# Kernel tuning notes

Hardware: AMD Instinct MI355X
Metric: run time of the kernel (lower is better)

## Reference

```python
import jax, jax.numpy as jnp
import numpy as np

NUM_NODES = 100000
NUM_EDGES = 1600000
FEAT = 128
HID = 128
NUM_GRAPHS = 512


def setup_inputs() -> dict:
    key = jax.random.key(0)
    ks = jax.random.split(key, 8)
    x = jax.random.normal(ks[0], (NUM_NODES, FEAT), dtype=jnp.float32)
    edge_index = jax.random.randint(ks[1], (2, NUM_EDGES), 0, NUM_NODES, dtype=jnp.int64)
    batch = jnp.sort(jax.random.randint(ks[2], (NUM_NODES,), 0, NUM_GRAPHS, dtype=jnp.int64))
    # Glorot-ish init for weights (scale named for clarity)
    s1 = 1.0 / np.sqrt(FEAT)
    s2 = 1.0 / np.sqrt(HID)
    W1 = jax.random.normal(ks[3], (FEAT, HID), dtype=jnp.float32) * s1
    b1 = jnp.zeros((HID,), dtype=jnp.float32)
    W2 = jax.random.normal(ks[4], (HID, HID), dtype=jnp.float32) * s2
    b2 = jnp.zeros((HID,), dtype=jnp.float32)
    Wout = jax.random.normal(ks[5], (HID, 1), dtype=jnp.float32) * s2
    bout = jnp.zeros((1,), dtype=jnp.float32)
    return {"x": x, "edge_index": edge_index, "batch": batch,
            "W1": W1, "b1": b1, "W2": W2, "b2": b2, "Wout": Wout, "bout": bout}


def reference(x, edge_index, batch, W1, b1, W2, b2, Wout, bout):
    N = x.shape[0]
    # PyG GCNConv: add self-loops, symmetric normalization D^-1/2 (A+I) D^-1/2
    loops = jnp.arange(N, dtype=edge_index.dtype)
    src = jnp.concatenate([edge_index[0], loops])  # [E+N]
    dst = jnp.concatenate([edge_index[1], loops])  # [E+N]
    ones = jnp.ones_like(dst, dtype=x.dtype)
    deg = jax.ops.segment_sum(ones, dst, num_segments=N)  # in-degree incl. self-loop
    dinv = jnp.where(deg > 0, jax.lax.rsqrt(deg), 0.0)
    coeff = (dinv[src] * dinv[dst])[:, None]  # [E+N, 1]

    def gcn(h, W, b):
        h = h @ W                                       # [N, H] dense GEMM
        msg = h[src] * coeff                            # gather + scale
        agg = jax.ops.segment_sum(msg, dst, num_segments=N)  # scatter-add
        return agg + b

    h = jax.nn.relu(gcn(x, W1, b1))
    h = jax.nn.relu(gcn(h, W2, b2))

    # global_mean_pool over batch ids
    G = NUM_GRAPHS
    sums = jax.ops.segment_sum(h, batch, num_segments=G)
    cnts = jax.ops.segment_sum(jnp.ones((N,), dtype=h.dtype), batch, num_segments=G)
    pooled = sums / jnp.maximum(cnts, 1.0)[:, None]

    return pooled @ Wout + bout  # [G, 1]
```

## Files before the change

kernel.cpp:

```cpp
#include <hip/hip_runtime.h>
#include <hip/hip_bf16.h>
#include <hip/hip_fp16.h>

#define FEAT 128
#define PSLOTS 64
#define BCAP 5120
#define NBIN 1024

typedef _Float16 h8 __attribute__((ext_vector_type(8)));
typedef float f4 __attribute__((ext_vector_type(4)));
typedef float fx2 __attribute__((ext_vector_type(2)));


__device__ __forceinline__ void wt_body(const float* __restrict__ W1,
                                        const float* __restrict__ W2,
                                        __half* __restrict__ Wt1,
                                        __half* __restrict__ Wt2, int bid) {
    int t = bid * 256 + threadIdx.x;
    const float* W = (t < 8192) ? W1 : W2;
    __half* Wt     = (t < 8192) ? Wt1 : Wt2;
    int u = t & 8191;
    int n = u >> 6, k2 = (u & 63) * 2;
    float a = W[(size_t)k2 * 128 + n];
    float b = W[(size_t)(k2 + 1) * 128 + n];
    ((__half2*)Wt)[n * 64 + (k2 >> 1)] = __floats2half2_rn(a, b);
}

__device__ __forceinline__ void bin_body(const int* __restrict__ ei, int E, int chunk,
                                         int* __restrict__ cursor,
                                         unsigned* __restrict__ binned, int nb,
                                         int bid, int* smem) {
    int* hist = smem;
    int* base = smem + 512;
    int start = bid * chunk;
    int end = start + chunk; if (end > E) end = E;
    for (int i = threadIdx.x; i < nb; i += 256) hist[i] = 0;
    __syncthreads();
    for (int e = start + threadIdx.x; e < end; e += 256)
        atomicAdd(&hist[ei[E + e] >> 8], 1);
    __syncthreads();
    for (int i = threadIdx.x; i < nb; i += 256) {
        int h = hist[i];
        base[i] = h ? atomicAdd(&cursor[i], h) : 0;
    }
    __syncthreads();
    for (int e = start + threadIdx.x; e < end; e += 256) {
        int s = ei[e];
        int d = ei[E + e];
        int b = d >> 8;
        int pos = atomicAdd(&base[b], 1);
        if (pos < BCAP)
            binned[(size_t)b * BCAP + pos] = (unsigned)s | ((unsigned)(d & 255) << 17);
    }
}

__global__ __launch_bounds__(256) void bin_wt(const int* __restrict__ ei, int E, int chunk,
                                              int* __restrict__ cursor,
                                              unsigned* __restrict__ binned, int nb,
                                              const float* __restrict__ W1,
                                              const float* __restrict__ W2,
                                              __half* __restrict__ Wt1,
                                              __half* __restrict__ Wt2) {
    __shared__ int smem[1024];
    if ((int)blockIdx.x < NBIN)
        bin_body(ei, E, chunk, cursor, binned, nb, blockIdx.x, smem);
    else
        wt_body(W1, W2, Wt1, Wt2, blockIdx.x - NBIN);
}


__device__ __forceinline__ void loadA(const __half* p, int quad, h8* a) {
#pragma unroll
    for (int ks = 0; ks < 4; ++ks)
        a[ks] = *(const h8*)(p + ks * 32 + quad * 8);
}
__device__ __forceinline__ void loadA(const float* p, int quad, h8* a) {
#pragma unroll
    for (int ks = 0; ks < 4; ++ks) {
        const float* q = p + ks * 32 + quad * 8;
        float4 f0 = *(const float4*)q;
        float4 f1 = *(const float4*)(q + 4);
        h8 v;
        v[0] = (_Float16)f0.x; v[1] = (_Float16)f0.y;
        v[2] = (_Float16)f0.z; v[3] = (_Float16)f0.w;
        v[4] = (_Float16)f1.x; v[5] = (_Float16)f1.y;
        v[6] = (_Float16)f1.z; v[7] = (_Float16)f1.w;
        a[ks] = v;
    }
}

template <typename TIN>
__device__ __forceinline__ void gemm_body(const TIN* __restrict__ X,
                                          const __half* __restrict__ Wt,
                                          unsigned char* __restrict__ Y, int N,
                                          const float* __restrict__ scale,
                                          int bid, _Float16* Bs) {
    {
        const float4* src = (const float4*)Wt;
        float4* dst = (float4*)Bs;
        for (int i = threadIdx.x; i < 2048; i += 256) {
            int n = i >> 4, ch = i & 15;
            dst[n * 16 + (ch ^ (n & 15))] = src[i];
        }
    }
    __syncthreads();

    int lane = threadIdx.x & 63;
    int wave = threadIdx.x >> 6;
    int m = lane & 15;
    int quad = lane >> 4;
    int rowb = bid * 128 + wave * 16;

    h8 a[2][4];
#pragma unroll
    for (int rt = 0; rt < 2; ++rt) {
        int rA = rowb + rt * 64 + m; if (rA >= N) rA = N - 1;
        loadA(X + (size_t)rA * FEAT, quad, a[rt]);
    }

    f4 acc[2][8];
#pragma unroll
    for (int rt = 0; rt < 2; ++rt)
#pragma unroll
        for (int nt = 0; nt < 8; ++nt) acc[rt][nt] = (f4){0.f, 0.f, 0.f, 0.f};

#pragma unroll
    for (int nt = 0; nt < 8; ++nt) {
        const _Float16* bbase = Bs + (nt * 16 + m) * 128;
#pragma unroll
        for (int ks = 0; ks < 4; ++ks) {
            int ch = (ks * 4 + quad) ^ m;
            h8 bfrag = *(const h8*)(bbase + ch * 8);
            acc[0][nt] = __builtin_amdgcn_mfma_f32_16x16x32_f16(a[0][ks], bfrag, acc[0][nt], 0, 0, 0);
            acc[1][nt] = __builtin_amdgcn_mfma_f32_16x16x32_f16(a[1][ks], bfrag, acc[1][nt], 0, 0, 0);
        }
    }

#pragma unroll
    for (int rt = 0; rt < 2; ++rt)
#pragma unroll
    for (int r = 0; r < 4; ++r) {
        int row = rowb + rt * 64 + quad * 4 + r;
        if (row < N) {
            float sc = scale[row];
#pragma unroll
            for (int nt = 0; nt < 8; ++nt) {
                float v = sc * acc[rt][nt][r];
                int pk = __builtin_amdgcn_cvt_pk_fp8_f32(v, v, 0, false);
                Y[(size_t)row * FEAT + nt * 16 + m] = (unsigned char)(pk & 0xFF);
            }
        }
    }
}

template <typename TIN>
__global__ __launch_bounds__(256) void gemm_mfma(const TIN* __restrict__ X,
                                                 const __half* __restrict__ Wt,
                                                 unsigned char* __restrict__ Y, int N,
                                                 const float* __restrict__ scale) {
    __shared__ __align__(16) _Float16 Bs[128 * 128];
    gemm_body<TIN>(X, Wt, Y, N, scale, blockIdx.x, Bs);
}


__global__ __launch_bounds__(256) void k_deg_fill(const unsigned* __restrict__ binned,
                                                  const int* __restrict__ cursor,
                                                  int N, int* __restrict__ deg,
                                                  int* __restrict__ rowstart,
                                                  float* __restrict__ dinv,
                                                  int* __restrict__ meta) {
    __shared__ int ld[256];
    __shared__ int sc[256];
    __shared__ int cur[256];
    int b = blockIdx.x;
    int cnt = cursor[b]; if (cnt > BCAP) cnt = BCAP;
    int s = b * BCAP, e = s + cnt;
    ld[threadIdx.x] = 0;
    __syncthreads();
    for (int i = s + threadIdx.x; i < e; i += 256)
        atomicAdd(&ld[binned[i] >> 17], 1);
    __syncthreads();
    int d = ld[threadIdx.x];
    sc[threadIdx.x] = d;
    __syncthreads();
    for (int off = 1; off < 256; off <<= 1) {
        int t = (threadIdx.x >= off) ? sc[threadIdx.x - off] : 0;
        __syncthreads();
        sc[threadIdx.x] += t;
        __syncthreads();
    }
    int rs = s + sc[threadIdx.x] - d;
    cur[threadIdx.x] = rs;
    int v = (b << 8) + threadIdx.x;
    if (v < N) {
        deg[v] = d;
        rowstart[v] = rs;
        dinv[v] = rsqrtf((float)d + 1.0f);
    }
    __syncthreads();
    for (int i = s + threadIdx.x; i < e; i += 256) {
        unsigned p = binned[i];
        int src = (int)(p & 0x1FFFF);
        int drl = (int)(p >> 17);
        int pos = atomicAdd(&cur[drl], 1);
        meta[pos] = src << 7;
    }
}


template <bool POOL>
__global__ __launch_bounds__(256) void agg_relu(const unsigned char* __restrict__ Y,
                                                const float* __restrict__ dinv,
                                                const int* __restrict__ rowstart,
                                                const int* __restrict__ degc,
                                                const int* __restrict__ meta,
                                                const float* __restrict__ bias,
                                                __half* __restrict__ H, int N,
                                                const float* __restrict__ Wout,
                                                const int* __restrict__ batch,
                                                float* __restrict__ gsum, int G) {
    int wid  = (blockIdx.x * 256 + threadIdx.x) >> 6;
    int lane = threadIdx.x & 63;
    if (wid >= N) return;
    int v = wid;
    float dv = dinv[v];
    int zoff = N << 7;

    const char* Yb = (const char*)Y;
    int lb = lane * 2;

    fx2 yv = __builtin_amdgcn_cvt_pk_f32_fp8(
        (int)*(const unsigned short*)(Y + (size_t)v * FEAT + lb), false);
    float accx = yv.x;
    float accy = yv.y;

    int base = rowstart[v];
    int n = degc[v];
    for (int i0 = 0; i0 < n; i0 += 64) {
        int m = n - i0; if (m > 64) m = 64;
        int sl = (lane < m) ? meta[base + i0 + lane] : zoff;
        for (int i = 0; i < m; i += 16) {
            int o[16];
            unsigned short u[16];
#pragma unroll
            for (int j = 0; j < 16; ++j) o[j] = __shfl(sl, i + j);
#pragma unroll
            for (int j = 0; j < 16; ++j)
                u[j] = *(const unsigned short*)(Yb + o[j] + lb);
#pragma unroll
            for (int j = 0; j < 16; ++j) {
                fx2 y = __builtin_amdgcn_cvt_pk_f32_fp8((int)u[j], false);
                accx += y.x;
                accy += y.y;
            }
        }
    }
    float2 b = ((const float2*)bias)[lane];
    float hx = fmaxf(dv * accx + b.x, 0.f);
    float hy = fmaxf(dv * accy + b.y, 0.f);
    if (POOL) {
        float2 wo = ((const float2*)Wout)[lane];
        float s = hx * wo.x + hy * wo.y;
        s += __shfl_xor(s, 1);
        s += __shfl_xor(s, 2);
        s += __shfl_xor(s, 4);
        s += __shfl_xor(s, 8);
        s += __shfl_xor(s, 16);
        s += __shfl_xor(s, 32);
        if (lane == 0) {
            int slot = blockIdx.x & (PSLOTS - 1);
            atomicAdd(&gsum[slot * G + batch[v]], s);
        }
    } else {
        ((__half2*)(H + (size_t)v * FEAT))[lane] = __floats2half2_rn(hx, hy);
    }
}


__global__ __launch_bounds__(256) void k_head(const float* __restrict__ gsum,
                                              const int* __restrict__ batch, int N, int G,
                                              const float* __restrict__ bout,
                                              float* __restrict__ out) {
    int g = blockIdx.x * 256 + threadIdx.x;
    if (g >= G) return;
    float s = 0.f;
#pragma unroll 8
    for (int k = 0; k < PSLOTS; ++k) s += gsum[k * G + g];
    int lo = 0, hi = N;
    while (lo < hi) { int mid = (lo + hi) >> 1; if (batch[mid] < g) lo = mid + 1; else hi = mid; }
    int start = lo;
    lo = start; hi = N;
    while (lo < hi) { int mid = (lo + hi) >> 1; if (batch[mid] < g + 1) lo = mid + 1; else hi = mid; }
    int cnt = lo - start;
    out[g] = s / (float)(cnt > 0 ? cnt : 1) + bout[0];
}


extern "C" void kernel_launch(void* const* d_in, const int* in_sizes, int n_in,
                              void* d_out, int out_size, void* d_ws, size_t ws_size,
                              hipStream_t stream) {
    const float* x    = (const float*)d_in[0];
    const int*   ei   = (const int*)d_in[1];
    const int*   batch= (const int*)d_in[2];
    const float* W1   = (const float*)d_in[3];
    const float* b1   = (const float*)d_in[4];
    const float* W2   = (const float*)d_in[5];
    const float* b2   = (const float*)d_in[6];
    const float* Wout = (const float*)d_in[7];
    const float* bout = (const float*)d_in[8];

    int N = in_sizes[0] / FEAT;
    int E = in_sizes[1] / 2;
    int G = out_size;
    int nb = (N + 255) >> 8;

    char* ws = (char*)d_ws;
    size_t off = 0;
    auto alloc = [&](size_t bytes) -> void* {
        void* p = ws + off;
        off += (bytes + 255) & ~(size_t)255;
        return p;
    };
    unsigned char* bufY = (unsigned char*)alloc((size_t)(N + 1) * FEAT);
    __half* bufH     = (__half*)alloc((size_t)N * FEAT * 2);
    __half* Wt1      = (__half*)alloc((size_t)FEAT * FEAT * 2);
    __half* Wt2      = (__half*)alloc((size_t)FEAT * FEAT * 2);
    float* dinv      = (float*)alloc((size_t)N * 4);
    int*   deg       = (int*)alloc((size_t)N * 4);
    int*   rowstart  = (int*)alloc((size_t)N * 4);
    float* gsum      = (float*)alloc((size_t)PSLOTS * G * 4 + (size_t)nb * 4);
    int*   cursor    = (int*)(gsum + (size_t)PSLOTS * G);
    unsigned* binned = (unsigned*)alloc((size_t)nb * BCAP * 4);
    int*   meta      = (int*)alloc((size_t)nb * BCAP * 4);

    int gemm_grid = (N + 127) / 128;
    int agg_grid  = (N + 3) / 4;
    int chunk = (E + NBIN - 1) / NBIN;

    hipMemsetAsync(gsum, 0, (size_t)PSLOTS * G * 4 + (size_t)nb * 4, stream);
    hipMemsetAsync(bufY + (size_t)N * FEAT, 0, FEAT, stream);
    bin_wt<<<NBIN + 64, 256, 0, stream>>>(ei, E, chunk, cursor, binned, nb,
                                          W1, W2, Wt1, Wt2);
    k_deg_fill<<<nb, 256, 0, stream>>>(binned, cursor, N, deg, rowstart, dinv, meta);
    gemm_mfma<float><<<gemm_grid, 256, 0, stream>>>(x, Wt1, bufY, N, dinv);
    agg_relu<false><<<agg_grid, 256, 0, stream>>>(bufY, dinv, rowstart, deg, meta, b1, bufH, N,
                                                  nullptr, nullptr, nullptr, 0);
    gemm_mfma<__half><<<gemm_grid, 256, 0, stream>>>(bufH, Wt2, bufY, N, dinv);
    agg_relu<true><<<agg_grid, 256, 0, stream>>>(bufY, dinv, rowstart, deg, meta, b2, nullptr, N,
                                                 Wout, batch, gsum, G);
    k_head<<<(G + 255) / 256, 256, 0, stream>>>(gsum, batch, N, G, bout, (float*)d_out);
}
```

Before: 290.7 us.

## Compute degrees with global atomics and overlap edge binning with first GEMM

A new pre-kernel computes node in-degrees with global atomics, transposes the weights and zeroes the padding row. This lets the first GEMM scale by rsqrt(deg+1) directly, so it runs in the same launch as edge binning and the two can overlap. k_deg_fill now reads deg instead of recounting per-bin histograms and pads meta with zero-row offsets. The aggregation kernel is restructured so four lane groups each gather 8-byte fp8 chunks for different neighbours and then reduce across groups with shuffles. The cost is one extra launch and a pass of global atomics over all edges.

```diff
diff --git a/kernel.cpp b/kernel.cpp
--- a/kernel.cpp
+++ b/kernel.cpp
@@ -6,6 +6,7 @@
 #define PSLOTS 64
 #define BCAP 5120
 #define NBIN 1024
+#define NDEG 1024
 
 typedef _Float16 h8 __attribute__((ext_vector_type(8)));
 typedef float f4 __attribute__((ext_vector_type(4)));
@@ -26,6 +27,27 @@
     ((__half2*)Wt)[n * 64 + (k2 >> 1)] = __floats2half2_rn(a, b);
 }
 
+
+__global__ __launch_bounds__(256) void k_pre(const int* __restrict__ ei, int E, int chunk,
+                                             int* __restrict__ deg,
+                                             const float* __restrict__ W1,
+                                             const float* __restrict__ W2,
+                                             __half* __restrict__ Wt1,
+                                             __half* __restrict__ Wt2,
+                                             unsigned char* __restrict__ padrow) {
+    int bid = blockIdx.x;
+    if (bid < NDEG) {
+        int start = bid * chunk;
+        int end = start + chunk; if (end > E) end = E;
+        for (int e = start + threadIdx.x; e < end; e += 256)
+            atomicAdd(&deg[ei[E + e]], 1);
+    } else if (bid < NDEG + 64) {
+        wt_body(W1, W2, Wt1, Wt2, bid - NDEG);
+    } else {
+        if (threadIdx.x < 8) ((uint4*)padrow)[threadIdx.x] = make_uint4(0, 0, 0, 0);
+    }
+}
+
 __device__ __forceinline__ void bin_body(const int* __restrict__ ei, int E, int chunk,
                                          int* __restrict__ cursor,
                                          unsigned* __restrict__ binned, int nb,
@@ -52,20 +74,6 @@
         if (pos < BCAP)
             binned[(size_t)b * BCAP + pos] = (unsigned)s | ((unsigned)(d & 255) << 17);
     }
-}
-
-__global__ __launch_bounds__(256) void bin_wt(const int* __restrict__ ei, int E, int chunk,
-                                              int* __restrict__ cursor,
-                                              unsigned* __restrict__ binned, int nb,
-                                              const float* __restrict__ W1,
-                                              const float* __restrict__ W2,
-                                              __half* __restrict__ Wt1,
-                                              __half* __restrict__ Wt2) {
-    __shared__ int smem[1024];
-    if ((int)blockIdx.x < NBIN)
-        bin_body(ei, E, chunk, cursor, binned, nb, blockIdx.x, smem);
-    else
-        wt_body(W1, W2, Wt1, Wt2, blockIdx.x - NBIN);
 }
 
 
@@ -93,7 +101,7 @@
 __device__ __forceinline__ void gemm_body(const TIN* __restrict__ X,
                                           const __half* __restrict__ Wt,
                                           unsigned char* __restrict__ Y, int N,
-                                          const float* __restrict__ scale,
+                                          const int* __restrict__ deg,
                                           int bid, _Float16* Bs) {
     {
         const float4* src = (const float4*)Wt;
@@ -142,7 +150,7 @@
     for (int r = 0; r < 4; ++r) {
         int row = rowb + rt * 64 + quad * 4 + r;
         if (row < N) {
-            float sc = scale[row];
+            float sc = rsqrtf((float)deg[row] + 1.0f);
 #pragma unroll
             for (int nt = 0; nt < 8; ++nt) {
                 float v = sc * acc[rt][nt][r];
@@ -153,34 +161,45 @@
     }
 }
 
+
+__global__ __launch_bounds__(256) void gemm_bin(const float* __restrict__ X,
+                                                const __half* __restrict__ Wt1,
+                                                unsigned char* __restrict__ Y,
+                                                const int* __restrict__ deg,
+                                                int N, int gemm_grid,
+                                                const int* __restrict__ ei, int E, int chunk,
+                                                int* __restrict__ cursor,
+                                                unsigned* __restrict__ binned, int nb) {
+    __shared__ __align__(16) char smem[32768];
+    if ((int)blockIdx.x < gemm_grid)
+        gemm_body<float>(X, Wt1, Y, N, deg, blockIdx.x, (_Float16*)smem);
+    else
+        bin_body(ei, E, chunk, cursor, binned, nb, blockIdx.x - gemm_grid, (int*)smem);
+}
+
+
 template <typename TIN>
 __global__ __launch_bounds__(256) void gemm_mfma(const TIN* __restrict__ X,
                                                  const __half* __restrict__ Wt,
-                                                 unsigned char* __restrict__ Y, int N,
-                                                 const float* __restrict__ scale) {
+                                                 unsigned char* __restrict__ Y,
+                                                 const int* __restrict__ deg, int N) {
     __shared__ __align__(16) _Float16 Bs[128 * 128];
-    gemm_body<TIN>(X, Wt, Y, N, scale, blockIdx.x, Bs);
+    gemm_body<TIN>(X, Wt, Y, N, deg, blockIdx.x, Bs);
 }
 
 
 __global__ __launch_bounds__(256) void k_deg_fill(const unsigned* __restrict__ binned,
                                                   const int* __restrict__ cursor,
-                                                  int N, int* __restrict__ deg,
-                                                  int* __restrict__ rowstart,
-                                                  float* __restrict__ dinv,
+                                                  const int* __restrict__ deg,
+                                                  int N, int* __restrict__ rowstart,
                                                   int* __restrict__ meta) {
-    __shared__ int ld[256];
     __shared__ int sc[256];
     __shared__ int cur[256];
     int b = blockIdx.x;
     int cnt = cursor[b]; if (cnt > BCAP) cnt = BCAP;
     int s = b * BCAP, e = s + cnt;
-    ld[threadIdx.x] = 0;
-    __syncthreads();
-    for (int i = s + threadIdx.x; i < e; i += 256)
-        atomicAdd(&ld[binned[i] >> 17], 1);
-    __syncthreads();
-    int d = ld[threadIdx.x];
+    int v = (b << 8) + threadIdx.x;
+    int d = (v < N) ? deg[v] : 0;
     sc[threadIdx.x] = d;
     __syncthreads();
     for (int off = 1; off < 256; off <<= 1) {
@@ -191,12 +210,7 @@
     }
     int rs = s + sc[threadIdx.x] - d;
     cur[threadIdx.x] = rs;
-    int v = (b << 8) + threadIdx.x;
-    if (v < N) {
-        deg[v] = d;
-        rowstart[v] = rs;
-        dinv[v] = rsqrtf((float)d + 1.0f);
-    }
+    if (v < N) rowstart[v] = rs;
     __syncthreads();
     for (int i = s + threadIdx.x; i < e; i += 256) {
         unsigned p = binned[i];
@@ -205,12 +219,23 @@
         int pos = atomicAdd(&cur[drl], 1);
         meta[pos] = src << 7;
     }
-}
-
+    int zoff = N << 7;
+    int t = cnt + threadIdx.x;
+    if (threadIdx.x < 64 && t < BCAP) meta[s + t] = zoff;
+}
+
+
+__device__ __forceinline__ void accum8(uint2 u, float* acc) {
+    fx2 p0 = __builtin_amdgcn_cvt_pk_f32_fp8((int)u.x, false);
+    fx2 p1 = __builtin_amdgcn_cvt_pk_f32_fp8((int)u.x, true);
+    fx2 p2 = __builtin_amdgcn_cvt_pk_f32_fp8((int)u.y, false);
+    fx2 p3 = __builtin_amdgcn_cvt_pk_f32_fp8((int)u.y, true);
+    acc[0] += p0.x; acc[1] += p0.y; acc[2] += p1.x; acc[3] += p1.y;
+    acc[4] += p2.x; acc[5] += p2.y; acc[6] += p3.x; acc[7] += p3.y;
+}
 
 template <bool POOL>
 __global__ __launch_bounds__(256) void agg_relu(const unsigned char* __restrict__ Y,
-                                                const float* __restrict__ dinv,
                                                 const int* __restrict__ rowstart,
                                                 const int* __restrict__ degc,
                                                 const int* __restrict__ meta,
@@ -223,56 +248,82 @@
     int lane = threadIdx.x & 63;
     if (wid >= N) return;
     int v = wid;
-    float dv = dinv[v];
+    int g = lane >> 4;
+    int c = lane & 15;
+    int cb = c * 8;
     int zoff = N << 7;
-
     const char* Yb = (const char*)Y;
-    int lb = lane * 2;
-
-    fx2 yv = __builtin_amdgcn_cvt_pk_f32_fp8(
-        (int)*(const unsigned short*)(Y + (size_t)v * FEAT + lb), false);
-    float accx = yv.x;
-    float accy = yv.y;
+
+    float acc[8];
+#pragma unroll
+    for (int k = 0; k < 8; ++k) acc[k] = 0.f;
+
+    {
+        int so = (g == 0) ? (v << 7) : zoff;
+        uint2 u = *(const uint2*)(Yb + so + cb);
+        accum8(u, acc);
+    }
 
     int base = rowstart[v];
     int n = degc[v];
-    for (int i0 = 0; i0 < n; i0 += 64) {
-        int m = n - i0; if (m > 64) m = 64;
-        int sl = (lane < m) ? meta[base + i0 + lane] : zoff;
-        for (int i = 0; i < m; i += 16) {
-            int o[16];
-            unsigned short u[16];
-#pragma unroll
-            for (int j = 0; j < 16; ++j) o[j] = __shfl(sl, i + j);
-#pragma unroll
-            for (int j = 0; j < 16; ++j)
-                u[j] = *(const unsigned short*)(Yb + o[j] + lb);
-#pragma unroll
-            for (int j = 0; j < 16; ++j) {
-                fx2 y = __builtin_amdgcn_cvt_pk_f32_fp8((int)u[j], false);
-                accx += y.x;
-                accy += y.y;
+    for (int i0 = 0; i0 < n; i0 += 32) {
+        int o[8];
+#pragma unroll
+        for (int j = 0; j < 8; ++j) {
+            int idx = i0 + g * 8 + j;
+            int mj = meta[base + idx];
+            o[j] = (idx < n) ? mj : zoff;
+        }
+        uint2 u[8];
+#pragma unroll
+        for (int j = 0; j < 8; ++j)
+            u[j] = *(const uint2*)(Yb + o[j] + cb);
+#pragma unroll
+        for (int j = 0; j < 8; ++j) accum8(u[j], acc);
+    }
+
+#pragma unroll
+    for (int k = 0; k < 8; ++k) {
+        acc[k] += __shfl_xor(acc[k], 16);
+        acc[k] += __shfl_xor(acc[k], 32);
+    }
+    float dv = rsqrtf((float)n + 1.0f);
+
+    if (POOL) {
+        const float4* bp = (const float4*)(bias + cb);
+        float4 b0 = bp[0], b1 = bp[1];
+        const float4* wp = (const float4*)(Wout + cb);
+        float4 w0 = wp[0], w1 = wp[1];
+        float h0 = fmaxf(dv * acc[0] + b0.x, 0.f);
+        float h1 = fmaxf(dv * acc[1] + b0.y, 0.f);
+        float h2 = fmaxf(dv * acc[2] + b0.z, 0.f);
+        float h3 = fmaxf(dv * acc[3] + b0.w, 0.f);
+        float h4 = fmaxf(dv * acc[4] + b1.x, 0.f);
+        float h5 = fmaxf(dv * acc[5] + b1.y, 0.f);
+        float h6 = fmaxf(dv * acc[6] + b1.z, 0.f);
+        float h7 = fmaxf(dv * acc[7] + b1.w, 0.f);
+        float s = h0 * w0.x + h1 * w0.y + h2 * w0.z + h3 * w0.w
+                + h4 * w1.x + h5 * w1.y + h6 * w1.z + h7 * w1.w;
+        if (g == 0) {
+            s += __shfl_xor(s, 1);
+            s += __shfl_xor(s, 2);
+            s += __shfl_xor(s, 4);
+            s += __shfl_xor(s, 8);
+            if (lane == 0) {
+                int slot = blockIdx.x & (PSLOTS - 1);
+                atomicAdd(&gsum[slot * G + batch[v]], s);
             }
         }
-    }
-    float2 b = ((const float2*)bias)[lane];
-    float hx = fmaxf(dv * accx + b.x, 0.f);
-    float hy = fmaxf(dv * accy + b.y, 0.f);
-    if (POOL) {
-        float2 wo = ((const float2*)Wout)[lane];
-        float s = hx * wo.x + hy * wo.y;
-        s += __shfl_xor(s, 1);
-        s += __shfl_xor(s, 2);
-        s += __shfl_xor(s, 4);
-        s += __shfl_xor(s, 8);
-        s += __shfl_xor(s, 16);
-        s += __shfl_xor(s, 32);
-        if (lane == 0) {
-            int slot = blockIdx.x & (PSLOTS - 1);
-            atomicAdd(&gsum[slot * G + batch[v]], s);
-        }
     } else {
-        ((__half2*)(H + (size_t)v * FEAT))[lane] = __floats2half2_rn(hx, hy);
+        float ax, ay;
+        if (g == 0)      { ax = acc[0]; ay = acc[1]; }
+        else if (g == 1) { ax = acc[2]; ay = acc[3]; }
+        else if (g == 2) { ax = acc[4]; ay = acc[5]; }
+        else             { ax = acc[6]; ay = acc[7]; }
+        float2 bb = *(const float2*)(bias + cb + g * 2);
+        float hx = fmaxf(dv * ax + bb.x, 0.f);
+        float hy = fmaxf(dv * ay + bb.y, 0.f);
+        *(__half2*)(H + (size_t)v * FEAT + cb + g * 2) = __floats2half2_rn(hx, hy);
     }
 }
 
@@ -325,28 +376,29 @@
     __half* bufH     = (__half*)alloc((size_t)N * FEAT * 2);
     __half* Wt1      = (__half*)alloc((size_t)FEAT * FEAT * 2);
     __half* Wt2      = (__half*)alloc((size_t)FEAT * FEAT * 2);
-    float* dinv      = (float*)alloc((size_t)N * 4);
-    int*   deg       = (int*)alloc((size_t)N * 4);
+    size_t zbytes    = (size_t)PSLOTS * G * 4 + (size_t)nb * 4 + (size_t)N * 4;
+    float* gsum      = (float*)alloc(zbytes);
+    int*   cursor    = (int*)(gsum + (size_t)PSLOTS * G);
+    int*   deg       = cursor + nb;
     int*   rowstart  = (int*)alloc((size_t)N * 4);
-    float* gsum      = (float*)alloc((size_t)PSLOTS * G * 4 + (size_t)nb * 4);
-    int*   cursor    = (int*)(gsum + (size_t)PSLOTS * G);
     unsigned* binned = (unsigned*)alloc((size_t)nb * BCAP * 4);
     int*   meta      = (int*)alloc((size_t)nb * BCAP * 4);
 
     int gemm_grid = (N + 127) / 128;
     int agg_grid  = (N + 3) / 4;
-    int chunk = (E + NBIN - 1) / NBIN;
-
-    hipMemsetAsync(gsum, 0, (size_t)PSLOTS * G * 4 + (size_t)nb * 4, stream);
-    hipMemsetAsync(bufY + (size_t)N * FEAT, 0, FEAT, stream);
-    bin_wt<<<NBIN + 64, 256, 0, stream>>>(ei, E, chunk, cursor, binned, nb,
-                                          W1, W2, Wt1, Wt2);
-    k_deg_fill<<<nb, 256, 0, stream>>>(binned, cursor, N, deg, rowstart, dinv, meta);
-    gemm_mfma<float><<<gemm_grid, 256, 0, stream>>>(x, Wt1, bufY, N, dinv);
-    agg_relu<false><<<agg_grid, 256, 0, stream>>>(bufY, dinv, rowstart, deg, meta, b1, bufH, N,
+    int chunkD = (E + NDEG - 1) / NDEG;
+    int chunkB = (E + NBIN - 1) / NBIN;
+
+    hipMemsetAsync(gsum, 0, zbytes, stream);
+    k_pre<<<NDEG + 65, 256, 0, stream>>>(ei, E, chunkD, deg, W1, W2, Wt1, Wt2,
+                                         bufY + (size_t)N * FEAT);
+    gemm_bin<<<gemm_grid + NBIN, 256, 0, stream>>>(x, Wt1, bufY, deg, N, gemm_grid,
+                                                   ei, E, chunkB, cursor, binned, nb);
+    k_deg_fill<<<nb, 256, 0, stream>>>(binned, cursor, deg, N, rowstart, meta);
+    agg_relu<false><<<agg_grid, 256, 0, stream>>>(bufY, rowstart, deg, meta, b1, bufH, N,
                                                   nullptr, nullptr, nullptr, 0);
-    gemm_mfma<__half><<<gemm_grid, 256, 0, stream>>>(bufH, Wt2, bufY, N, dinv);
-    agg_relu<true><<<agg_grid, 256, 0, stream>>>(bufY, dinv, rowstart, deg, meta, b2, nullptr, N,
+    gemm_mfma<__half><<<gemm_grid, 256, 0, stream>>>(bufH, Wt2, bufY, deg, N);
+    agg_relu<true><<<agg_grid, 256, 0, stream>>>(bufY, rowstart, deg, meta, b2, nullptr, N,
                                                  Wout, batch, gsum, G);
     k_head<<<(G + 255) / 256, 256, 0, stream>>>(gsum, batch, N, G, bout, (float*)d_out);
 }
```

New measurement: 342.1 us. 1.18x slower.
